# Optimization experiments

Hardware: AMD Instinct MI355X
Metric: run time of the kernel (lower is better)

Reference implementation:

```python
import jax, jax.numpy as jnp
import numpy as np

HEADS = 12
ROT_DIM = 16  # hidden_dim // num_heads // 4
MAX_FREQ = 256
EPS = 1e-5


def _groupnorm(x, w, b, groups, eps=EPS):
    # x: [B, C, H, W, D]; normalize per (group, H, W, D)
    B, C = x.shape[0], x.shape[1]
    xr = x.reshape(B, groups, -1)
    mu = xr.mean(-1, keepdims=True)
    var = xr.var(-1, keepdims=True)
    xn = ((xr - mu) * jax.lax.rsqrt(var + eps)).reshape(x.shape)
    return xn * w.reshape(1, C, 1, 1, 1) + b.reshape(1, C, 1, 1, 1)


def _layernorm(t, w, b, eps=EPS):
    mu = t.mean(-1, keepdims=True)
    var = t.var(-1, keepdims=True)
    return (t - mu) * jax.lax.rsqrt(var + eps) * w + b


def _rotate_half(t):
    # pairs adjacent elements: (x1, x2) -> (-x2, x1)
    x1 = t[..., 0::2]
    x2 = t[..., 1::2]
    return jnp.stack([-x2, x1], axis=-1).reshape(t.shape)


def _axial_freqs(H, W, D, dim=ROT_DIM, max_freq=MAX_FREQ):
    # 'pixel' rotary: base freqs = linspace(1, max_freq/2, dim//2) * pi, pos in [-1, 1]
    base = jnp.linspace(1.0, max_freq / 2.0, dim // 2) * jnp.pi

    def ax(n):
        pos = jnp.linspace(-1.0, 1.0, n)
        f = pos[:, None] * base[None, :]          # [n, dim//2]
        return jnp.repeat(f, 2, axis=-1)           # [n, dim]

    fh = jnp.broadcast_to(ax(H)[:, None, None, :], (H, W, D, dim))
    fw = jnp.broadcast_to(ax(W)[None, :, None, :], (H, W, D, dim))
    fd = jnp.broadcast_to(ax(D)[None, None, :, :], (H, W, D, dim))
    return jnp.concatenate([fh, fw, fd], -1)       # [H, W, D, 3*dim]


def _rope(freqs, t):
    # t: [B, he, H, W, D, hd]; rotate first rot dims, pass rest through
    rot = freqs.shape[-1]
    tl, tr = t[..., :rot], t[..., rot:]
    tl = tl * jnp.cos(freqs) + _rotate_half(tl) * jnp.sin(freqs)
    return jnp.concatenate([tl, tr], -1)


def setup_inputs() -> dict:
    key = jax.random.key(0)
    ks = jax.random.split(key, 14)
    B, C, H, W, D = 2, 768, 16, 16, 8
    hd = C // HEADS
    f32 = jnp.float32
    inp = {
        "x": jax.random.normal(ks[0], (B, C, H, W, D), f32),
        "norm1_w": 1.0 + 0.1 * jax.random.normal(ks[1], (C,), f32),
        "norm1_b": 0.1 * jax.random.normal(ks[2], (C,), f32),
        "gamma_att": 0.01 * jnp.ones((C,), f32),
        "W_fused": jax.random.normal(ks[3], (C, 7 * C), f32) / np.sqrt(C),
        "b_fused": 0.01 * jax.random.normal(ks[4], (7 * C,), f32),
        "qn_w": 1.0 + 0.1 * jax.random.normal(ks[5], (hd,), f32),
        "qn_b": 0.1 * jax.random.normal(ks[6], (hd,), f32),
        "kn_w": 1.0 + 0.1 * jax.random.normal(ks[7], (hd,), f32),
        "kn_b": 0.1 * jax.random.normal(ks[8], (hd,), f32),
        "W_attn": jax.random.normal(ks[9], (C, C), f32) / np.sqrt(C),
        "W_ffout": jax.random.normal(ks[10], (2 * C, C), f32) / np.sqrt(2 * C),
        "b_ffout": 0.01 * jax.random.normal(ks[11], (C,), f32),
        "bcs": 0,
        "axis_order": 0,
    }
    return inp


def reference(x, norm1_w, norm1_b, gamma_att, W_fused, b_fused, qn_w, qn_b,
              kn_w, kn_b, W_attn, W_ffout, b_ffout, bcs, axis_order):
    B, C, H, W, D = x.shape
    he = HEADS
    hd = C // he
    x_in = x

    # GroupNorm over channels (num_groups = num_heads)
    xn = _groupnorm(x, norm1_w, norm1_b, he)
    t = jnp.transpose(xn, (0, 2, 3, 4, 1))             # b h w d c

    fused = t @ W_fused + b_fused                      # b h w d 7C
    ff, q, k, v = jnp.split(fused, [4 * C, 5 * C, 6 * C], axis=-1)

    def to_heads(z):
        return z.reshape(B, H, W, D, he, hd).transpose(0, 4, 1, 2, 3, 5)  # b he h w d c

    q, k, v = to_heads(q), to_heads(k), to_heads(v)
    q = _layernorm(q, qn_w, qn_b)
    k = _layernorm(k, kn_w, kn_b)

    freqs = _axial_freqs(H, W, D)                      # [H, W, D, 48]
    q = _rope(freqs, q)
    k = _rope(freqs, k)

    S = H * W * D
    qf = q.reshape(B, he, S, hd)
    kf = k.reshape(B, he, S, hd)
    vf = v.reshape(B, he, S, hd)

    scale = 1.0 / np.sqrt(hd)
    scores = jnp.einsum('bhqc,bhkc->bhqk', qf, kf) * scale
    attn = jax.nn.softmax(scores, axis=-1)
    out = jnp.einsum('bhqk,bhkc->bhqc', attn, vf)      # b he S hd

    att = out.reshape(B, he, H, W, D, hd).transpose(0, 2, 3, 4, 1, 5).reshape(B, H, W, D, C)
    att_out = att @ W_attn

    # SwiGLU: first half is value, second half gates
    xh, gate = jnp.split(ff, 2, axis=-1)
    ff_out = (jax.nn.silu(gate) * xh) @ W_ffout + b_ffout

    y = gamma_att * (att_out + ff_out)                 # b h w d c
    return jnp.transpose(y, (0, 4, 1, 2, 3)) + x_in    # b c h w d
```

## Files before the change

### kernel.cpp

```cpp
#include <hip/hip_runtime.h>
#include <hip/hip_bf16.h>

#define HE   12
#define HD   64
#define Cc   768
#define C2   1536
#define C4   3072
#define N7   5376
#define Bb   2
#define Ss   2048
#define BSr  4096
#define PI_F 3.14159265358979f

using f32x4  = __attribute__((ext_vector_type(4))) float;
using short8 = __attribute__((ext_vector_type(8))) short;

__device__ __forceinline__ unsigned short f2b(float f) {
    union { float f; unsigned int u; } v; v.f = f;
    unsigned int u = v.u;
    unsigned int r = (u + 0x7fffu + ((u >> 16) & 1u)) >> 16;
    return (unsigned short)r;
}
__device__ __forceinline__ unsigned short f2bt(float f) {
    union { float f; unsigned int u; } v; v.f = f;
    return (unsigned short)(v.u >> 16);
}
__device__ __forceinline__ float b2f(unsigned short s) {
    union { unsigned int u; float f; } v; v.u = ((unsigned int)s) << 16;
    return v.f;
}
__device__ __forceinline__ f32x4 mfma16(short8 a, short8 b, f32x4 c) {
    return __builtin_amdgcn_mfma_f32_16x16x32_bf16(a, b, c, 0, 0, 0);
}
__device__ __forceinline__ void gl_lds16(const unsigned short* g, unsigned short* l) {
    __builtin_amdgcn_global_load_lds(
        (const __attribute__((address_space(1))) unsigned int*)(const void*)g,
        (__attribute__((address_space(3))) unsigned int*)(void*)l, 16, 0, 0);
}
__device__ __forceinline__ void xcd_tile(int& bx, int& by) {
    int nx = gridDim.x;
    int flat = blockIdx.y * nx + blockIdx.x;
    int nwg = nx * gridDim.y;
    int swz = (flat & 7) * (nwg >> 3) + (flat >> 3);
    bx = swz % nx; by = swz / nx;
}

union U8 { uint4 v; unsigned short u[8]; };

__global__ __launch_bounds__(256) void transpose_w(const float* __restrict__ src,
                                                   unsigned short* __restrict__ dst,
                                                   int R, int Ccol) {
    __shared__ float tile[32][33];
    int tx = threadIdx.x & 31, ty = threadIdx.x >> 5;
    int rt = blockIdx.y * 32, ct = blockIdx.x * 32;
#pragma unroll
    for (int i = 0; i < 4; ++i)
        tile[ty + i * 8][tx] = src[(size_t)(rt + ty + i * 8) * Ccol + ct + tx];
    __syncthreads();
#pragma unroll
    for (int i = 0; i < 4; ++i)
        dst[(size_t)(ct + ty + i * 8) * R + rt + tx] = f2b(tile[tx][ty + i * 8]);
}

__global__ __launch_bounds__(256) void gn_stats(const float* __restrict__ x,
                                                float* __restrict__ stat) {
    int j = blockIdx.x;
    const float4* p = (const float4*)(x + (size_t)j * 131072);
    float s = 0.f, ss = 0.f;
    for (int i = threadIdx.x; i < 32768; i += 256) {
        float4 v = p[i];
        s  += v.x + v.y + v.z + v.w;
        ss += v.x * v.x + v.y * v.y + v.z * v.z + v.w * v.w;
    }
#pragma unroll
    for (int m = 1; m < 64; m <<= 1) { s += __shfl_xor(s, m); ss += __shfl_xor(ss, m); }
    __shared__ float ls[4], lss[4];
    int wid = threadIdx.x >> 6;
    if ((threadIdx.x & 63) == 0) { ls[wid] = s; lss[wid] = ss; }
    __syncthreads();
    if (threadIdx.x == 0) {
        s = ls[0] + ls[1] + ls[2] + ls[3];
        ss = lss[0] + lss[1] + lss[2] + lss[3];
        float mu  = s / 131072.0f;
        float var = ss / 131072.0f - mu * mu;
        stat[j * 2]     = mu;
        stat[j * 2 + 1] = rsqrtf(var + 1e-5f);
    }
}

__global__ __launch_bounds__(256) void norm_transpose(const float* __restrict__ x,
                                                      const float* __restrict__ stat,
                                                      const float* __restrict__ w,
                                                      const float* __restrict__ bgn,
                                                      unsigned short* __restrict__ t) {
    __shared__ float tile[32][33];
    int b = blockIdx.z;
    int st = blockIdx.x * 32, ct = blockIdx.y * 32;
    int tx = threadIdx.x & 31, ty = threadIdx.x >> 5;
#pragma unroll
    for (int i = 0; i < 4; ++i) {
        int c = ct + ty + i * 8;
        int g = c >> 6;
        float mu = stat[(b * 12 + g) * 2], rs = stat[(b * 12 + g) * 2 + 1];
        float v = x[(size_t)(b * Cc + c) * Ss + st + tx];
        tile[ty + i * 8][tx] = (v - mu) * rs * w[c] + bgn[c];
    }
    __syncthreads();
#pragma unroll
    for (int i = 0; i < 4; ++i) {
        int s = st + ty + i * 8, c = ct + tx;
        t[(size_t)(b * Ss + s) * Cc + c] = f2b(tile[tx][ty + i * 8]);
    }
}

template<bool ACCUM, bool BIAS, bool OUTBF16>
__global__ __launch_bounds__(256) void gemm128(const unsigned short* __restrict__ A,
                                               const unsigned short* __restrict__ Bt,
                                               const float* __restrict__ bias,
                                               void* __restrict__ Cout,
                                               int M, int N, int K) {
    __shared__ __align__(16) unsigned short As[2][128 * 32];
    __shared__ __align__(16) unsigned short Bs[2][128 * 32];
    const int tid = threadIdx.x;
    const int wid = tid >> 6, lane = tid & 63;
    const int lr = lane & 15, lh = lane >> 4;
    const int wr = wid >> 1, wc = wid & 1;
    int bx, by; xcd_tile(bx, by);
    const int row0 = by * 128, col0 = bx * 128;
    const int srow = tid >> 2;
    const int kcs  = (((tid & 3) ^ ((tid >> 3) & 3)) * 8);
    const unsigned short* ga = A  + (size_t)(row0 + srow) * K + kcs;
    const unsigned short* gb = Bt + (size_t)(col0 + srow) * K + kcs;
    const int csw = ((lr >> 1) & 3) << 3;
    f32x4 acc[4][4] = {};

    auto STAGE = [&](int buf, int k0) {
        gl_lds16(ga + k0,          &As[buf][tid * 8]);
        gl_lds16(ga + 64 * K + k0, &As[buf][2048 + tid * 8]);
        gl_lds16(gb + k0,          &Bs[buf][tid * 8]);
        gl_lds16(gb + 64 * K + k0, &Bs[buf][2048 + tid * 8]);
    };

    STAGE(0, 0);
    __syncthreads();
    for (int k0 = 0; k0 < K; k0 += 32) {
        const int cur = (k0 >> 5) & 1;
        if (k0 + 32 < K) STAGE(cur ^ 1, k0 + 32);
        short8 af[4], bfr[4];
#pragma unroll
        for (int m = 0; m < 4; ++m)
            af[m]  = *(const short8*)&As[cur][(wr * 64 + m * 16 + lr) * 32 + ((lh << 3) ^ csw)];
#pragma unroll
        for (int n = 0; n < 4; ++n)
            bfr[n] = *(const short8*)&Bs[cur][(wc * 64 + n * 16 + lr) * 32 + ((lh << 3) ^ csw)];
#pragma unroll
        for (int m = 0; m < 4; ++m)
#pragma unroll
            for (int n = 0; n < 4; ++n)
                acc[m][n] = mfma16(af[m], bfr[n], acc[m][n]);
        __syncthreads();
    }

#pragma unroll
    for (int m = 0; m < 4; ++m)
#pragma unroll
        for (int n = 0; n < 4; ++n) {
            int row = row0 + wr * 64 + m * 16 + lh * 4;
            int col = col0 + wc * 64 + n * 16 + lr;
            float bv = BIAS ? bias[col] : 0.0f;
#pragma unroll
            for (int r = 0; r < 4; ++r) {
                size_t idx = (size_t)(row + r) * N + col;
                float v = acc[m][n][r] + bv;
                if (ACCUM) v += ((const float*)Cout)[idx];
                if (OUTBF16) ((unsigned short*)Cout)[idx] = f2b(v);
                else         ((float*)Cout)[idx] = v;
            }
        }
}

__global__ __launch_bounds__(256) void gemm_fin(const unsigned short* __restrict__ A,
                                                const unsigned short* __restrict__ Bt,
                                                const float* __restrict__ bo,
                                                const float* __restrict__ oaccIn,
                                                const float* __restrict__ x,
                                                const float* __restrict__ gamma,
                                                float* __restrict__ out,
                                                int M, int N, int K) {
    __shared__ __align__(16) unsigned short As[2][128 * 32];
    __shared__ __align__(16) unsigned short Bs[2][128 * 32];
    const int tid = threadIdx.x;
    const int wid = tid >> 6, lane = tid & 63;
    const int lr = lane & 15, lh = lane >> 4;
    const int wr = wid >> 1, wc = wid & 1;
    int bx, by; xcd_tile(bx, by);
    const int row0 = by * 128, col0 = bx * 128;
    const int srow = tid >> 2;
    const int kcs  = (((tid & 3) ^ ((tid >> 3) & 3)) * 8);
    const unsigned short* ga = A  + (size_t)(row0 + srow) * K + kcs;
    const unsigned short* gb = Bt + (size_t)(col0 + srow) * K + kcs;
    const int csw = ((lr >> 1) & 3) << 3;
    f32x4 acc[4][4] = {};

    auto STAGE = [&](int buf, int k0) {
        gl_lds16(ga + k0,          &As[buf][tid * 8]);
        gl_lds16(ga + 64 * K + k0, &As[buf][2048 + tid * 8]);
        gl_lds16(gb + k0,          &Bs[buf][tid * 8]);
        gl_lds16(gb + 64 * K + k0, &Bs[buf][2048 + tid * 8]);
    };

    STAGE(0, 0);
    __syncthreads();
    for (int k0 = 0; k0 < K; k0 += 32) {
        const int cur = (k0 >> 5) & 1;
        if (k0 + 32 < K) STAGE(cur ^ 1, k0 + 32);
        short8 af[4], bfr[4];
#pragma unroll
        for (int m = 0; m < 4; ++m)
            af[m]  = *(const short8*)&As[cur][(wr * 64 + m * 16 + lr) * 32 + ((lh << 3) ^ csw)];
#pragma unroll
        for (int n = 0; n < 4; ++n)
            bfr[n] = *(const short8*)&Bs[cur][(wc * 64 + n * 16 + lr) * 32 + ((lh << 3) ^ csw)];
#pragma unroll
        for (int m = 0; m < 4; ++m)
#pragma unroll
            for (int n = 0; n < 4; ++n)
                acc[m][n] = mfma16(af[m], bfr[n], acc[m][n]);
        __syncthreads();
    }

#pragma unroll
    for (int m = 0; m < 4; ++m)
#pragma unroll
        for (int n = 0; n < 4; ++n) {
            int row = row0 + wr * 64 + m * 16 + lh * 4;
            int col = col0 + wc * 64 + n * 16 + lr;
            float bv = bo[col], gv = gamma[col];
#pragma unroll
            for (int r = 0; r < 4; ++r) {
                int rw = row + r;
                float v = acc[m][n][r] + bv + oaccIn[(size_t)rw * N + col];
                int b = rw >> 11, s = rw & 2047;
                size_t oidx = (size_t)(b * Cc + col) * Ss + s;
                out[oidx] = gv * v + x[oidx];
            }
        }
}

__global__ __launch_bounds__(256) void qkv_prep(const unsigned short* __restrict__ fused,
                                                const float* __restrict__ qnw, const float* __restrict__ qnb,
                                                const float* __restrict__ knw, const float* __restrict__ knb,
                                                unsigned short* __restrict__ qf,
                                                unsigned short* __restrict__ kf,
                                                unsigned short* __restrict__ vf) {
    const int wid = threadIdx.x >> 6, lane = threadIdx.x & 63;
    const int job = blockIdx.x * 4 + wid;
    const int srow = job / 12, h = job % 12;
    const int b = srow >> 11, s = srow & 2047;

    size_t base = (size_t)srow * N7 + C4 + h * HD;
    float qv = b2f(fused[base + lane]);
    float kv = b2f(fused[base + Cc + lane]);
    float vv = b2f(fused[base + 2 * Cc + lane]);

    float qs = qv, ks = kv;
#pragma unroll
    for (int m = 1; m < 64; m <<= 1) { qs += __shfl_xor(qs, m); ks += __shfl_xor(ks, m); }
    float qmu = qs * (1.0f / 64.0f), kmu = ks * (1.0f / 64.0f);
    float qd = qv - qmu, kd = kv - kmu;
    float qv2 = qd * qd, kv2 = kd * kd;
#pragma unroll
    for (int m = 1; m < 64; m <<= 1) { qv2 += __shfl_xor(qv2, m); kv2 += __shfl_xor(kv2, m); }
    float qn = qd * rsqrtf(qv2 * (1.0f / 64.0f) + 1e-5f) * qnw[lane] + qnb[lane];
    float kn = kd * rsqrtf(kv2 * (1.0f / 64.0f) + 1e-5f) * knw[lane] + knb[lane];

    if (lane < 48) {
        int axis = lane >> 4, ii = (lane & 15) >> 1;
        float basef = (1.0f + (float)ii * (127.0f / 7.0f)) * PI_F;
        int   pos_i = (axis == 0) ? (s >> 7) : (axis == 1) ? ((s >> 3) & 15) : (s & 7);
        float denom = (axis == 2) ? 7.0f : 15.0f;
        float pos   = -1.0f + 2.0f * (float)pos_i / denom;
        float ang   = pos * basef;
        float sn, cs;
        sincosf(ang, &sn, &cs);
        float qp = __shfl_xor(qn, 1);
        float kp = __shfl_xor(kn, 1);
        qn = (lane & 1) ? (qn * cs + qp * sn) : (qn * cs - qp * sn);
        kn = (lane & 1) ? (kn * cs + kp * sn) : (kn * cs - kp * sn);
    }

    size_t obase = ((size_t)(b * 12 + h) * Ss + s) * HD + lane;
    qf[obase] = f2b(qn);
    kf[obase] = f2b(kn);
    vf[obase] = f2b(vv);
}

__global__ __launch_bounds__(256) void ffa_prep(const unsigned short* __restrict__ fused,
                                                unsigned short* __restrict__ ffa) {
    int i8 = blockIdx.x * 256 + threadIdx.x;
    int row = i8 / 192, co = (i8 % 192) * 8;
    U8 xa, ga, oa;
    xa.v = *(const uint4*)&fused[(size_t)row * N7 + co];
    ga.v = *(const uint4*)&fused[(size_t)row * N7 + C2 + co];
#pragma unroll
    for (int j = 0; j < 8; ++j) {
        float g = b2f(ga.u[j]);
        float xh = b2f(xa.u[j]);
        float sg = 1.0f / (1.0f + __expf(-g));
        oa.u[j] = f2b(g * sg * xh);
    }
    *(uint4*)&ffa[(size_t)row * C2 + co] = oa.v;
}

__global__ __launch_bounds__(256) void attn64(const unsigned short* __restrict__ qf,
                                              const unsigned short* __restrict__ kf,
                                              const unsigned short* __restrict__ vf,
                                              float* __restrict__ opart) {
    __shared__ __align__(16) unsigned short Ks[64][72];
    __shared__ __align__(16) unsigned short Vt[64][72];
    __shared__ __align__(16) unsigned short Ps[4][16][72];
    const int tid = threadIdx.x, wid = tid >> 6, lane = tid & 63;
    const int lr = lane & 15, lh = lane >> 4;
    const int bh = blockIdx.y, qt = blockIdx.x, half = blockIdx.z;
    const size_t kvbase = (size_t)bh * Ss * HD;

    const int qrow = qt * 64 + wid * 16 + lr;
    short8 qa0 = *(const short8*)&qf[kvbase + (size_t)qrow * HD + lh * 8];
    short8 qa1 = *(const short8*)&qf[kvbase + (size_t)qrow * HD + 32 + lh * 8];

    const int r0 = tid >> 3, kc0 = (tid & 7) * 8;
    const int sv0 = (((r0 >> 3) ^ (kc0 >> 3)) << 3) | (r0 & 7);
    const int sv1 = ((((r0 >> 3) + 4) ^ (kc0 >> 3)) << 3) | (r0 & 7);
    const unsigned short* kptr = kf + kvbase + (size_t)(half * 16 * 64 + r0) * HD + kc0;
    const unsigned short* vptr = vf + kvbase + (size_t)(half * 16 * 64 + r0) * HD + kc0;

    const short8 ones = {0x3F80, 0x3F80, 0x3F80, 0x3F80, 0x3F80, 0x3F80, 0x3F80, 0x3F80};
    const float c1 = 0.125f * 1.44269504f;
    const float c2 = 23.08312065f;
    const int rxb = (lr >> 2) & 3;

    f32x4 oacc[4] = {};
    f32x4 lacc = {};

    uint4 kreg0 = *(const uint4*)kptr;
    uint4 kreg1 = *(const uint4*)(kptr + 32 * HD);
    U8 vreg0, vreg1;
    vreg0.v = *(const uint4*)vptr;
    vreg1.v = *(const uint4*)(vptr + 32 * HD);

    for (int kt = 0; kt < 16; ++kt) {
        *(uint4*)&Ks[r0][kc0]      = kreg0;
        *(uint4*)&Ks[r0 + 32][kc0] = kreg1;
#pragma unroll
        for (int j = 0; j < 8; ++j) Vt[kc0 + j][sv0] = vreg0.u[j];
#pragma unroll
        for (int j = 0; j < 8; ++j) Vt[kc0 + j][sv1] = vreg1.u[j];
        __syncthreads();

        if (kt < 15) {
            const unsigned short* kp = kptr + (size_t)(kt + 1) * 64 * HD;
            const unsigned short* vp = vptr + (size_t)(kt + 1) * 64 * HD;
            kreg0   = *(const uint4*)kp;
            kreg1   = *(const uint4*)(kp + 32 * HD);
            vreg0.v = *(const uint4*)vp;
            vreg1.v = *(const uint4*)(vp + 32 * HD);
        }

        f32x4 sc[4];
#pragma unroll
        for (int n = 0; n < 4; ++n) {
            f32x4 z = {0.f, 0.f, 0.f, 0.f};
            short8 k0 = *(const short8*)&Ks[n * 16 + lr][lh * 8];
            short8 k1 = *(const short8*)&Ks[n * 16 + lr][32 + lh * 8];
            z = mfma16(qa0, k0, z);
            z = mfma16(qa1, k1, z);
            sc[n] = z;
        }

#pragma unroll
        for (int n = 0; n < 4; ++n)
#pragma unroll
            for (int r = 0; r < 4; ++r)
                sc[n][r] = exp2f(sc[n][r] * c1 - c2);

#pragma unroll
        for (int r = 0; r < 4; ++r) {
            int prow = lh * 4 + r;
            int lo = lr & 7, lr3 = lr >> 3;
            Ps[wid][prow][(((0 + lr3) ^ lh) << 3) | lo] = f2bt(sc[0][r]);
            Ps[wid][prow][(((2 + lr3) ^ lh) << 3) | lo] = f2bt(sc[1][r]);
            Ps[wid][prow][(((4 + lr3) ^ lh) << 3) | lo] = f2bt(sc[2][r]);
            Ps[wid][prow][(((6 + lr3) ^ lh) << 3) | lo] = f2bt(sc[3][r]);
        }

        short8 pa0 = *(const short8*)&Ps[wid][lr][((lh ^ rxb) & 7) * 8];
        short8 pa1 = *(const short8*)&Ps[wid][lr][(((lh + 4) ^ rxb) & 7) * 8];
        lacc = mfma16(pa0, ones, lacc);
        lacc = mfma16(pa1, ones, lacc);
#pragma unroll
        for (int n = 0; n < 4; ++n) {
            int dv = (2 * n + (lr >> 3)) & 7;
            short8 v0 = *(const short8*)&Vt[n * 16 + lr][((lh ^ dv) & 7) * 8];
            short8 v1 = *(const short8*)&Vt[n * 16 + lr][(((lh + 4) ^ dv) & 7) * 8];
            oacc[n] = mfma16(pa0, v0, oacc[n]);
            oacc[n] = mfma16(pa1, v1, oacc[n]);
        }
        __syncthreads();
    }

    const size_t cb = ((size_t)((bh * 32 + qt) * 2 + half)) * 4160;
#pragma unroll
    for (int n = 0; n < 4; ++n)
#pragma unroll
        for (int r = 0; r < 4; ++r)
            opart[cb + (size_t)(wid * 16 + lh * 4 + r) * 64 + n * 16 + lr] = oacc[n][r];
    if (lr == 0)
#pragma unroll
        for (int r = 0; r < 4; ++r)
            opart[cb + 4096 + wid * 16 + lh * 4 + r] = lacc[r];
}

__global__ __launch_bounds__(256) void att_combine(const float* __restrict__ opart,
                                                   unsigned short* __restrict__ att) {
    int i = blockIdx.x * 256 + threadIdx.x;
    int d4 = i & 15, q = (i >> 4) & 63, qt = (i >> 10) & 31, bh = i >> 15;
    size_t cb = ((size_t)(bh * 32 + qt) * 2) * 4160;
    float4 o0 = *(const float4*)&opart[cb + (size_t)q * 64 + d4 * 4];
    float4 o1 = *(const float4*)&opart[cb + 4160 + (size_t)q * 64 + d4 * 4];
    float rl = 1.0f / (opart[cb + 4096 + q] + opart[cb + 4160 + 4096 + q]);
    int b = bh / 12, h = bh % 12;
    size_t row = (size_t)(b * Ss + qt * 64 + q);
    ushort4 w;
    w.x = f2b((o0.x + o1.x) * rl);
    w.y = f2b((o0.y + o1.y) * rl);
    w.z = f2b((o0.z + o1.z) * rl);
    w.w = f2b((o0.w + o1.w) * rl);
    *(ushort4*)&att[row * Cc + h * HD + d4 * 4] = w;
}

extern "C" void kernel_launch(void* const* d_in, const int* in_sizes, int n_in,
                              void* d_out, int out_size, void* d_ws, size_t ws_size,
                              hipStream_t stream) {
    const float* x     = (const float*)d_in[0];
    const float* n1w   = (const float*)d_in[1];
    const float* n1b   = (const float*)d_in[2];
    const float* gamma = (const float*)d_in[3];
    const float* Wf    = (const float*)d_in[4];
    const float* bfu   = (const float*)d_in[5];
    const float* qnw   = (const float*)d_in[6];
    const float* qnb   = (const float*)d_in[7];
    const float* knw   = (const float*)d_in[8];
    const float* knb   = (const float*)d_in[9];
    const float* Wa    = (const float*)d_in[10];
    const float* Wo    = (const float*)d_in[11];
    const float* bo    = (const float*)d_in[12];

    char* ws = (char*)d_ws;
    size_t off = 0;
    auto alloc = [&](size_t bytes) {
        char* p = ws + off;
        off = (off + bytes + 255) & ~(size_t)255;
        return p;
    };
    float*          stat  = (float*)alloc(24 * 2 * 4);
    unsigned short* t     = (unsigned short*)alloc((size_t)BSr * Cc * 2);
    unsigned short* WtF   = (unsigned short*)alloc((size_t)N7 * Cc * 2);
    unsigned short* fused = (unsigned short*)alloc((size_t)BSr * N7 * 2);
    unsigned short* qfB   = (unsigned short*)alloc((size_t)Bb * HE * Ss * HD * 2);
    unsigned short* kfB   = (unsigned short*)alloc((size_t)Bb * HE * Ss * HD * 2);
    unsigned short* vfB   = (unsigned short*)alloc((size_t)Bb * HE * Ss * HD * 2);
    unsigned short* ffa   = (unsigned short*)alloc((size_t)BSr * C2 * 2);
    unsigned short* WtA   = (unsigned short*)alloc((size_t)Cc * Cc * 2);
    unsigned short* WtO   = (unsigned short*)alloc((size_t)Cc * C2 * 2);
    unsigned short* attB  = t;
    float*          oacc  = (float*)fused;
    float*          opart = oacc + (size_t)BSr * Cc;

    transpose_w<<<dim3(N7 / 32, Cc / 32), 256, 0, stream>>>(Wf, WtF, Cc, N7);
    transpose_w<<<dim3(Cc / 32, Cc / 32), 256, 0, stream>>>(Wa, WtA, Cc, Cc);
    transpose_w<<<dim3(Cc / 32, C2 / 32), 256, 0, stream>>>(Wo, WtO, C2, Cc);

    gn_stats<<<24, 256, 0, stream>>>(x, stat);
    norm_transpose<<<dim3(Ss / 32, Cc / 32, Bb), 256, 0, stream>>>(x, stat, n1w, n1b, t);

    gemm128<false, true, true><<<dim3(N7 / 128, BSr / 128), 256, 0, stream>>>(
        t, WtF, bfu, fused, BSr, N7, Cc);

    qkv_prep<<<(Bb * Ss * HE) / 4, 256, 0, stream>>>(fused, qnw, qnb, knw, knb, qfB, kfB, vfB);
    ffa_prep<<<(BSr * C2 / 8) / 256, 256, 0, stream>>>(fused, ffa);

    attn64<<<dim3(Ss / 64, Bb * HE, 2), 256, 0, stream>>>(qfB, kfB, vfB, opart);
    att_combine<<<3072, 256, 0, stream>>>(opart, attB);

    gemm128<false, false, false><<<dim3(Cc / 128, BSr / 128), 256, 0, stream>>>(
        attB, WtA, nullptr, oacc, BSr, Cc, Cc);
    gemm_fin<<<dim3(Cc / 128, BSr / 128), 256, 0, stream>>>(
        ffa, WtO, bo, oacc, x, gamma, (float*)d_out, BSr, Cc, C2);
}
```

Before: 380.1 us.

## Pre-transpose V, double-buffer K/V via direct global-to-LDS loads, drop split-K combine

V is now transposed once into a [bh][d][s] layout by a new kernel, so the attention kernel no longer scatters V into a transposed LDS tile. K and V tiles are loaded straight into double-buffered, XOR-swizzled LDS with gl_lds16, and the next tile is staged while MFMAs run on the current one; setprio hints favour the MFMA sections. The key-split across two blocks and the separate combine kernel are removed, so each block covers all 32 key tiles and normalises and writes bf16 output itself. This removes the fp32 partial-result round trip and one launch, at the cost of half as many attention blocks and one extra transpose pass.

Result: faster. 372.6 us (-2.0%).

```diff
diff --git a/kernel.cpp b/kernel.cpp
--- a/kernel.cpp
+++ b/kernel.cpp
@@ -251,8 +251,7 @@
                                                 const float* __restrict__ qnw, const float* __restrict__ qnb,
                                                 const float* __restrict__ knw, const float* __restrict__ knb,
                                                 unsigned short* __restrict__ qf,
-                                                unsigned short* __restrict__ kf,
-                                                unsigned short* __restrict__ vf) {
+                                                unsigned short* __restrict__ kf) {
     const int wid = threadIdx.x >> 6, lane = threadIdx.x & 63;
     const int job = blockIdx.x * 4 + wid;
     const int srow = job / 12, h = job % 12;
@@ -261,7 +260,6 @@
     size_t base = (size_t)srow * N7 + C4 + h * HD;
     float qv = b2f(fused[base + lane]);
     float kv = b2f(fused[base + Cc + lane]);
-    float vv = b2f(fused[base + 2 * Cc + lane]);
 
     float qs = qv, ks = kv;
 #pragma unroll
@@ -292,7 +290,31 @@
     size_t obase = ((size_t)(b * 12 + h) * Ss + s) * HD + lane;
     qf[obase] = f2b(qn);
     kf[obase] = f2b(kn);
-    vf[obase] = f2b(vv);
+}
+
+__global__ __launch_bounds__(256) void v_transpose(const unsigned short* __restrict__ fused,
+                                                   unsigned short* __restrict__ vt) {
+    __shared__ unsigned short tile[64][72];
+    const int tid = threadIdx.x;
+    const int bh = blockIdx.y, st = blockIdx.x * 64;
+    const int b = bh / 12, h = bh % 12;
+    const size_t src0 = (size_t)(b * Ss + st) * N7 + C4 + 2 * Cc + h * HD;
+#pragma unroll
+    for (int j = 0; j < 2; ++j) {
+        int e = j * 256 + tid;
+        int sr = e >> 3, c8 = (e & 7) * 8;
+        *(uint4*)&tile[sr][c8] = *(const uint4*)&fused[src0 + (size_t)sr * N7 + c8];
+    }
+    __syncthreads();
+#pragma unroll
+    for (int j = 0; j < 2; ++j) {
+        int e = j * 256 + tid;
+        int d = e >> 3, s8 = (e & 7) * 8;
+        U8 o;
+#pragma unroll
+        for (int jj = 0; jj < 8; ++jj) o.u[jj] = tile[s8 + jj][d];
+        *(uint4*)&vt[((size_t)bh * HD + d) * Ss + st + s8] = o.v;
+    }
 }
 
 __global__ __launch_bounds__(256) void ffa_prep(const unsigned short* __restrict__ fused,
@@ -314,68 +336,63 @@
 
 __global__ __launch_bounds__(256) void attn64(const unsigned short* __restrict__ qf,
                                               const unsigned short* __restrict__ kf,
-                                              const unsigned short* __restrict__ vf,
-                                              float* __restrict__ opart) {
-    __shared__ __align__(16) unsigned short Ks[64][72];
-    __shared__ __align__(16) unsigned short Vt[64][72];
+                                              const unsigned short* __restrict__ vt,
+                                              unsigned short* __restrict__ att) {
+    __shared__ __align__(16) unsigned short Ks[2][64 * 64];
+    __shared__ __align__(16) unsigned short Vs[2][64 * 64];
     __shared__ __align__(16) unsigned short Ps[4][16][72];
     const int tid = threadIdx.x, wid = tid >> 6, lane = tid & 63;
     const int lr = lane & 15, lh = lane >> 4;
-    const int bh = blockIdx.y, qt = blockIdx.x, half = blockIdx.z;
-    const size_t kvbase = (size_t)bh * Ss * HD;
+    const int bh = blockIdx.y, qt = blockIdx.x;
+    const int b = bh / 12, h = bh % 12;
+    const size_t kbase = (size_t)bh * Ss * HD;
+    const size_t vbase = (size_t)bh * HD * Ss;
 
     const int qrow = qt * 64 + wid * 16 + lr;
-    short8 qa0 = *(const short8*)&qf[kvbase + (size_t)qrow * HD + lh * 8];
-    short8 qa1 = *(const short8*)&qf[kvbase + (size_t)qrow * HD + 32 + lh * 8];
-
-    const int r0 = tid >> 3, kc0 = (tid & 7) * 8;
-    const int sv0 = (((r0 >> 3) ^ (kc0 >> 3)) << 3) | (r0 & 7);
-    const int sv1 = ((((r0 >> 3) + 4) ^ (kc0 >> 3)) << 3) | (r0 & 7);
-    const unsigned short* kptr = kf + kvbase + (size_t)(half * 16 * 64 + r0) * HD + kc0;
-    const unsigned short* vptr = vf + kvbase + (size_t)(half * 16 * 64 + r0) * HD + kc0;
+    short8 qa0 = *(const short8*)&qf[kbase + (size_t)qrow * HD + lh * 8];
+    short8 qa1 = *(const short8*)&qf[kbase + (size_t)qrow * HD + 32 + lh * 8];
+
+    const int r0  = wid * 16 + (lane >> 3);
+    const int sc0 = ((lane & 7) ^ (lane >> 3)) * 8;
+    const unsigned short* ksrc = kf + kbase + (size_t)r0 * HD + sc0;
+    const unsigned short* vsrc = vt + vbase + (size_t)r0 * Ss + sc0;
+    const int ldst = wid * 1024 + lane * 8;
 
     const short8 ones = {0x3F80, 0x3F80, 0x3F80, 0x3F80, 0x3F80, 0x3F80, 0x3F80, 0x3F80};
     const float c1 = 0.125f * 1.44269504f;
     const float c2 = 23.08312065f;
     const int rxb = (lr >> 2) & 3;
+    const int xr  = lr & 7;
 
     f32x4 oacc[4] = {};
     f32x4 lacc = {};
 
-    uint4 kreg0 = *(const uint4*)kptr;
-    uint4 kreg1 = *(const uint4*)(kptr + 32 * HD);
-    U8 vreg0, vreg1;
-    vreg0.v = *(const uint4*)vptr;
-    vreg1.v = *(const uint4*)(vptr + 32 * HD);
-
-    for (int kt = 0; kt < 16; ++kt) {
-        *(uint4*)&Ks[r0][kc0]      = kreg0;
-        *(uint4*)&Ks[r0 + 32][kc0] = kreg1;
-#pragma unroll
-        for (int j = 0; j < 8; ++j) Vt[kc0 + j][sv0] = vreg0.u[j];
-#pragma unroll
-        for (int j = 0; j < 8; ++j) Vt[kc0 + j][sv1] = vreg1.u[j];
-        __syncthreads();
-
-        if (kt < 15) {
-            const unsigned short* kp = kptr + (size_t)(kt + 1) * 64 * HD;
-            const unsigned short* vp = vptr + (size_t)(kt + 1) * 64 * HD;
-            kreg0   = *(const uint4*)kp;
-            kreg1   = *(const uint4*)(kp + 32 * HD);
-            vreg0.v = *(const uint4*)vp;
-            vreg1.v = *(const uint4*)(vp + 32 * HD);
-        }
+    auto STAGE = [&](int buf, int kt) {
+        gl_lds16(ksrc + (size_t)(kt * 64) * HD,          &Ks[buf][ldst]);
+        gl_lds16(ksrc + (size_t)(kt * 64 + 8) * HD,      &Ks[buf][ldst + 512]);
+        gl_lds16(vsrc + kt * 64,                         &Vs[buf][ldst]);
+        gl_lds16(vsrc + kt * 64 + 8 * Ss,                &Vs[buf][ldst + 512]);
+    };
+
+    STAGE(0, 0);
+    __syncthreads();
+
+    for (int kt = 0; kt < 32; ++kt) {
+        const int cur = kt & 1;
+        if (kt < 31) STAGE(cur ^ 1, kt + 1);
 
         f32x4 sc[4];
+        __builtin_amdgcn_s_setprio(1);
 #pragma unroll
         for (int n = 0; n < 4; ++n) {
             f32x4 z = {0.f, 0.f, 0.f, 0.f};
-            short8 k0 = *(const short8*)&Ks[n * 16 + lr][lh * 8];
-            short8 k1 = *(const short8*)&Ks[n * 16 + lr][32 + lh * 8];
+            short8 k0 = *(const short8*)&Ks[cur][(n * 16 + lr) * 64 + ((lh ^ xr) & 7) * 8];
+            short8 k1 = *(const short8*)&Ks[cur][(n * 16 + lr) * 64 + (((lh + 4) ^ xr) & 7) * 8];
             z = mfma16(qa0, k0, z);
             z = mfma16(qa1, k1, z);
             sc[n] = z;
         }
+        __builtin_amdgcn_s_setprio(0);
 
 #pragma unroll
         for (int n = 0; n < 4; ++n)
@@ -395,47 +412,31 @@
 
         short8 pa0 = *(const short8*)&Ps[wid][lr][((lh ^ rxb) & 7) * 8];
         short8 pa1 = *(const short8*)&Ps[wid][lr][(((lh + 4) ^ rxb) & 7) * 8];
+        __builtin_amdgcn_s_setprio(1);
         lacc = mfma16(pa0, ones, lacc);
         lacc = mfma16(pa1, ones, lacc);
 #pragma unroll
         for (int n = 0; n < 4; ++n) {
-            int dv = (2 * n + (lr >> 3)) & 7;
-            short8 v0 = *(const short8*)&Vt[n * 16 + lr][((lh ^ dv) & 7) * 8];
-            short8 v1 = *(const short8*)&Vt[n * 16 + lr][(((lh + 4) ^ dv) & 7) * 8];
+            short8 v0 = *(const short8*)&Vs[cur][(n * 16 + lr) * 64 + ((lh ^ xr) & 7) * 8];
+            short8 v1 = *(const short8*)&Vs[cur][(n * 16 + lr) * 64 + (((lh + 4) ^ xr) & 7) * 8];
             oacc[n] = mfma16(pa0, v0, oacc[n]);
             oacc[n] = mfma16(pa1, v1, oacc[n]);
         }
+        __builtin_amdgcn_s_setprio(0);
         __syncthreads();
     }
 
-    const size_t cb = ((size_t)((bh * 32 + qt) * 2 + half)) * 4160;
+    float rinv[4];
+#pragma unroll
+    for (int r = 0; r < 4; ++r) rinv[r] = 1.0f / lacc[r];
 #pragma unroll
     for (int n = 0; n < 4; ++n)
 #pragma unroll
-        for (int r = 0; r < 4; ++r)
-            opart[cb + (size_t)(wid * 16 + lh * 4 + r) * 64 + n * 16 + lr] = oacc[n][r];
-    if (lr == 0)
-#pragma unroll
-        for (int r = 0; r < 4; ++r)
-            opart[cb + 4096 + wid * 16 + lh * 4 + r] = lacc[r];
-}
-
-__global__ __launch_bounds__(256) void att_combine(const float* __restrict__ opart,
-                                                   unsigned short* __restrict__ att) {
-    int i = blockIdx.x * 256 + threadIdx.x;
-    int d4 = i & 15, q = (i >> 4) & 63, qt = (i >> 10) & 31, bh = i >> 15;
-    size_t cb = ((size_t)(bh * 32 + qt) * 2) * 4160;
-    float4 o0 = *(const float4*)&opart[cb + (size_t)q * 64 + d4 * 4];
-    float4 o1 = *(const float4*)&opart[cb + 4160 + (size_t)q * 64 + d4 * 4];
-    float rl = 1.0f / (opart[cb + 4096 + q] + opart[cb + 4160 + 4096 + q]);
-    int b = bh / 12, h = bh % 12;
-    size_t row = (size_t)(b * Ss + qt * 64 + q);
-    ushort4 w;
-    w.x = f2b((o0.x + o1.x) * rl);
-    w.y = f2b((o0.y + o1.y) * rl);
-    w.z = f2b((o0.z + o1.z) * rl);
-    w.w = f2b((o0.w + o1.w) * rl);
-    *(ushort4*)&att[row * Cc + h * HD + d4 * 4] = w;
+        for (int r = 0; r < 4; ++r) {
+            int srow_w = qt * 64 + wid * 16 + lh * 4 + r;
+            int col = h * HD + n * 16 + lr;
+            att[(size_t)(b * Ss + srow_w) * Cc + col] = f2b(oacc[n][r] * rinv[r]);
+        }
 }
 
 extern "C" void kernel_launch(void* const* d_in, const int* in_sizes, int n_in,
@@ -468,13 +469,12 @@
     unsigned short* fused = (unsigned short*)alloc((size_t)BSr * N7 * 2);
     unsigned short* qfB   = (unsigned short*)alloc((size_t)Bb * HE * Ss * HD * 2);
     unsigned short* kfB   = (unsigned short*)alloc((size_t)Bb * HE * Ss * HD * 2);
-    unsigned short* vfB   = (unsigned short*)alloc((size_t)Bb * HE * Ss * HD * 2);
+    unsigned short* vtB   = (unsigned short*)alloc((size_t)Bb * HE * Ss * HD * 2);
     unsigned short* ffa   = (unsigned short*)alloc((size_t)BSr * C2 * 2);
     unsigned short* WtA   = (unsigned short*)alloc((size_t)Cc * Cc * 2);
     unsigned short* WtO   = (unsigned short*)alloc((size_t)Cc * C2 * 2);
     unsigned short* attB  = t;
     float*          oacc  = (float*)fused;
-    float*          opart = oacc + (size_t)BSr * Cc;
 
     transpose_w<<<dim3(N7 / 32, Cc / 32), 256, 0, stream>>>(Wf, WtF, Cc, N7);
     transpose_w<<<dim3(Cc / 32, Cc / 32), 256, 0, stream>>>(Wa, WtA, Cc, Cc);
@@ -486,11 +486,11 @@
     gemm128<false, true, true><<<dim3(N7 / 128, BSr / 128), 256, 0, stream>>>(
         t, WtF, bfu, fused, BSr, N7, Cc);
 
-    qkv_prep<<<(Bb * Ss * HE) / 4, 256, 0, stream>>>(fused, qnw, qnb, knw, knb, qfB, kfB, vfB);
+    qkv_prep<<<(Bb * Ss * HE) / 4, 256, 0, stream>>>(fused, qnw, qnb, knw, knb, qfB, kfB);
+    v_transpose<<<dim3(Ss / 64, Bb * HE), 256, 0, stream>>>(fused, vtB);
     ffa_prep<<<(BSr * C2 / 8) / 256, 256, 0, stream>>>(fused, ffa);
 
-    attn64<<<dim3(Ss / 64, Bb * HE, 2), 256, 0, stream>>>(qfB, kfB, vfB, opart);
-    att_combine<<<3072, 256, 0, stream>>>(opart, attB);
+    attn64<<<dim3(Ss / 64, Bb * HE), 256, 0, stream>>>(qfB, kfB, vtB, attB);
 
     gemm128<false, false, false><<<dim3(Cc / 128, BSr / 128), 256, 0, stream>>>(
         attB, WtA, nullptr, oacc, BSr, Cc, Cc);
```
